# Optimization experiments

Measured on AMD Instinct MI355X. Metric: run time of the kernel, lower is better.

Reference implementation:

```python
import jax, jax.numpy as jnp
import numpy as np

T_INF = 10
LR_R = 0.02
EPS = 1e-5

def conv(x, w):
    # torch F.conv2d, padding=1, OIHW weights, NCHW data
    return jax.lax.conv_general_dilated(x, w, (1, 1), ((1, 1), (1, 1)),
                                        dimension_numbers=('NCHW', 'OIHW', 'NCHW'))

def convT(x, w):
    # torch ConvTranspose2d (stride=1, padding=1), weight layout (Cin, Cout, kH, kW)
    # equivalent to conv with spatially-flipped, channel-swapped kernel
    wc = jnp.flip(w, (2, 3)).transpose(1, 0, 2, 3)
    return conv(x, wc)

def maxpool2(x):
    return jax.lax.reduce_window(x, -jnp.inf, jax.lax.max, (1, 1, 2, 2), (1, 1, 2, 2), 'VALID')

def avgpool2(x):
    return jax.lax.reduce_window(x, 0.0, jax.lax.add, (1, 1, 2, 2), (1, 1, 2, 2), 'VALID') * 0.25

def bn(x, g, b):
    # BatchNorm2d in training mode (batch statistics, biased variance), eps=1e-5
    m = x.mean((0, 2, 3), keepdims=True)
    v = x.var((0, 2, 3), keepdims=True)
    return (x - m) * jax.lax.rsqrt(v + EPS) * g[None, :, None, None] + b[None, :, None, None]

def up2(x):
    return jnp.repeat(jnp.repeat(x, 2, axis=2), 2, axis=3)

def setup_inputs() -> dict:
    key = jax.random.key(0)
    B, C1, C2, C3 = 256, 64, 128, 256
    ks = jax.random.split(key, 12)
    def w(k, shape, fan_in):
        return jax.random.normal(k, shape, jnp.float32) * (1.0 / np.sqrt(fan_in))
    return {
        'x':  jax.random.normal(ks[0], (B, 3, 32, 32), jnp.float32),
        'W1': w(ks[1], (C1, 3, 3, 3), 3 * 9),
        'W2': w(ks[2], (C2, C1, 3, 3), C1 * 9),
        'W3': w(ks[3], (C3, C2, 3, 3), C2 * 9),
        'P2': w(ks[4], (C2, C1, 3, 3), C2 * 9),  # ConvTranspose2d(C2, C1) weight layout
        'P3': w(ks[5], (C3, C2, 3, 3), C3 * 9),  # ConvTranspose2d(C3, C2) weight layout
        'g1': jnp.ones((C1,), jnp.float32), 'b1': jnp.zeros((C1,), jnp.float32),
        'g2': jnp.ones((C2,), jnp.float32), 'b2': jnp.zeros((C2,), jnp.float32),
        'g3': jnp.ones((C3,), jnp.float32), 'b3': jnp.zeros((C3,), jnp.float32),
    }

def reference(x, W1, W2, W3, P2, P3, g1, b1, g2, b2, g3, b3):
    # feed-forward initialization
    r1 = maxpool2(jax.nn.relu(bn(conv(x, W1), g1, b1)))   # [B,C1,16,16]
    r2 = maxpool2(jax.nn.relu(bn(conv(r1, W2), g2, b2)))  # [B,C2,8,8]
    r3 = maxpool2(jax.nn.relu(bn(conv(r2, W3), g3, b3)))  # [B,C3,4,4]
    # iterative predictive-coding inference
    for _ in range(T_INF):
        pred1 = jnp.tanh(up2(convT(r2, P2)))  # P2(r2) is 8x8, upsample to 16x16
        pred2 = jnp.tanh(up2(convT(r3, P3)))  # P3(r3) is 4x4, upsample to 8x8
        e1 = r1 - pred1
        e2 = r2 - pred2
        dr1 = -e1
        dr2 = -e2 + avgpool2(conv(e1, W2))
        dr3 = avgpool2(conv(e2, W3))
        r1 = jax.nn.relu(r1 + LR_R * dr1)
        r2 = jax.nn.relu(r2 + LR_R * dr2)
        r3 = jax.nn.relu(r3 + LR_R * dr3)
    return (r1, r2, r3)
```

## Files before the change

kernel.cpp:

```cpp
#include <hip/hip_runtime.h>
#include <cstddef>
#include <cstdint>

#define LRr 0.02f

typedef unsigned short u16;
typedef __attribute__((ext_vector_type(8))) __bf16 bf16x8;
typedef __attribute__((ext_vector_type(8))) short short8;
typedef __attribute__((ext_vector_type(4))) float f32x4;
typedef __attribute__((ext_vector_type(4))) u16 u16x4;

static __device__ __forceinline__ u16 f2bf(float f) {
  union { float f; unsigned int u; } v{f};
  unsigned int r = (v.u + 0x7FFFu + ((v.u >> 16) & 1u)) >> 16;
  return (u16)r;
}
static __device__ __forceinline__ float bf2f(u16 h) {
  union { unsigned int u; float f; } v{(unsigned int)h << 16};
  return v.f;
}

static __device__ __forceinline__ void gload_lds16(const void* g, void* l) {
  __builtin_amdgcn_global_load_lds(
      (const __attribute__((address_space(1))) unsigned int*)g,
      (__attribute__((address_space(3))) unsigned int*)l, 16, 0, 0);
}

enum { EP_RAW = 0, EP_E1 = 1, EP_E2 = 2, EP_P2 = 3, EP_P3 = 4 };

template<int H, int CIN, int COUT, int WAVES_M, int WAVES_N, int WM, int WN,
         int NBLK, int EPI, bool SPLIT_M, bool STATS>
__device__ __forceinline__ void gemm_body(
    int bid, char* lds,
    const u16* __restrict__ in, const u16* __restrict__ wpk,
    float* __restrict__ fout, u16* __restrict__ bout,
    const u16* __restrict__ aux, float* __restrict__ sums)
{
  constexpr int P = H * H, W = H;
  constexpr int LW = (H == 16) ? 4 : ((H == 8) ? 3 : 2);
  constexpr int M_rep = WM / 16, N_rep = WN / 16;
  constexpr int CCH = CIN / 32;
  constexpr int PW = H + 2;
  constexpr int ALDS = PW * PW * CIN * 2;
  constexpr int COB = WAVES_N * WN;
  constexpr int BSTEP = 32 * COB * 2;
  constexpr int NS = 9 * CCH;
  static_assert(SPLIT_M ? (WAVES_M * WM * NBLK == P) : (WAVES_M * WM == P), "M");
  static_assert(SPLIT_M ? (COB == COUT) : (COB * NBLK == COUT), "N");
  static_assert(ALDS + 2 * BSTEP <= 64 * 1024, "lds");

  const int tid = threadIdx.x;
  const int l = tid & 63, l15 = l & 15, lq = l >> 4;
  const int wid = tid >> 6;
  const int wn = wid % WAVES_N, wm = wid / WAVES_N;

  const int img  = (NBLK == 1) ? bid : bid / NBLK;
  const int half = (NBLK == 1) ? 0 : bid % NBLK;
  const int pix0 = SPLIT_M ? half * (WAVES_M * WM) : 0;
  const int co0b = SPLIT_M ? 0 : half * COB;
  const int wm0  = pix0 + wm * WM;
  const int co   = co0b + wn * WN;

  auto stageB = [&](int buf, int step) {
    constexpr int ROUNDS = (4 * COB) / 256;
#pragma unroll
    for (int r = 0; r < ROUNDS; ++r) {
      int j = r * 256 + tid;
      int g = j / COB, c = j % COB;
      const char* gp = (const char*)wpk + ((size_t)((step * 4 + g) * COUT + co0b + c) << 4);
      char* lp = lds + ALDS + buf * BSTEP + ((r * 256 + (tid & 192)) << 4);
      gload_lds16(gp, lp);
    }
  };

  stageB(0, 0);
  for (int i = tid * 16; i < ALDS; i += 4096)
    *(int4*)(lds + i) = make_int4(0, 0, 0, 0);
  __syncthreads();
  constexpr int NCH = P * CIN / 8;
  for (int i = tid; i < NCH; i += 256) {
    int pix = i / (CIN / 8), c8 = i % (CIN / 8);
    const char* gp = (const char*)in + (((size_t)img * P + pix) * CIN + c8 * 8) * 2;
    int cell = ((pix >> LW) + 1) * PW + (pix & (W - 1)) + 1;
    int lb = ((cell * CIN + c8 * 8) << 1) ^ ((cell & 7) << 4);
    *(short8*)(lds + lb) = *(const short8*)gp;
  }
  __syncthreads();

  f32x4 acc[M_rep][N_rep];
#pragma unroll
  for (int m = 0; m < M_rep; ++m)
#pragma unroll
    for (int n = 0; n < N_rep; ++n)
#pragma unroll
      for (int r = 0; r < 4; ++r) acc[m][n][r] = 0.f;

  int ym[M_rep], xm[M_rep];
#pragma unroll
  for (int m = 0; m < M_rep; ++m) {
    int pix = wm0 + m * 16 + l15;
    ym[m] = pix >> LW;
    xm[m] = pix & (W - 1);
  }

  int step = 0, buf = 0;
  for (int tap = 0; tap < 9; ++tap) {
    const int dy = tap / 3, dx = tap % 3;
    for (int cc = 0; cc < CCH; ++cc) {
      if (step + 1 < NS) stageB(buf ^ 1, step + 1);
      bf16x8 af[M_rep], bfr[N_rep];
#pragma unroll
      for (int m = 0; m < M_rep; ++m) {
        int cell = (ym[m] + dy) * PW + xm[m] + dx;
        int lb = ((cell * CIN + cc * 32 + lq * 8) << 1) ^ ((cell & 7) << 4);
        af[m] = *(const bf16x8*)(lds + lb);
      }
#pragma unroll
      for (int n = 0; n < N_rep; ++n) {
        int lb = (lq * COB + wn * WN + n * 16 + l15) << 4;
        bfr[n] = *(const bf16x8*)(lds + ALDS + buf * BSTEP + lb);
      }
#pragma unroll
      for (int m = 0; m < M_rep; ++m)
#pragma unroll
        for (int n = 0; n < N_rep; ++n)
          acc[m][n] = __builtin_amdgcn_mfma_f32_16x16x32_bf16(af[m], bfr[n], acc[m][n], 0, 0, 0);
      __syncthreads();
      buf ^= 1;
      ++step;
    }
  }

  if constexpr (STATS) {
    float* sbuf = (float*)lds;
    for (int i = tid; i < 2 * COB; i += 256) sbuf[i] = 0.f;
    __syncthreads();
#pragma unroll
    for (int n = 0; n < N_rep; ++n) {
      float s1 = 0.f, s2 = 0.f;
#pragma unroll
      for (int m = 0; m < M_rep; ++m)
#pragma unroll
        for (int r = 0; r < 4; ++r) {
          float v = acc[m][n][r];
          s1 += v; s2 += v * v;
        }
      s1 += __shfl_xor(s1, 16); s2 += __shfl_xor(s2, 16);
      s1 += __shfl_xor(s1, 32); s2 += __shfl_xor(s2, 32);
      if (lq == 0) {
        int cg = wn * WN + n * 16 + l15;
        atomicAdd(&sbuf[2 * cg], s1);
        atomicAdd(&sbuf[2 * cg + 1], s2);
      }
    }
    __syncthreads();
    for (int i = tid; i < 2 * COB; i += 256) atomicAdd(&sums[2 * co0b + i], sbuf[i]);
  }

  const int gyx = 0; (void)gyx;

  if constexpr (EPI == EP_RAW) {
#pragma unroll
    for (int m = 0; m < M_rep; ++m)
#pragma unroll
      for (int n = 0; n < N_rep; ++n)
#pragma unroll
        for (int r = 0; r < 4; ++r) {
          int pix = wm0 + m * 16 + lq * 4 + r;
          bout[((size_t)img * P + pix) * COUT + co + n * 16 + l15] = f2bf(acc[m][n][r]);
        }
  } else if constexpr (EPI == EP_E1) {
#pragma unroll
    for (int m = 0; m < M_rep; ++m)
#pragma unroll
      for (int n = 0; n < N_rep; ++n)
#pragma unroll
        for (int r = 0; r < 4; ++r) {
          int pix = wm0 + m * 16 + lq * 4 + r;
          int y = pix >> 3, x = pix & 7;
          int cg = co + n * 16 + l15;
          float t = tanhf(acc[m][n][r]);
#pragma unroll
          for (int d2 = 0; d2 < 4; ++d2) {
            size_t idx = ((size_t)img * 256 + (2 * y + (d2 >> 1)) * 16 + 2 * x + (d2 & 1)) * 64 + cg;
            float rv = fout[idx];
            float e = rv - t;
            bout[idx] = f2bf(e);
            fout[idx] = fmaxf(rv - LRr * e, 0.f);
          }
        }
  } else if constexpr (EPI == EP_E2) {
#pragma unroll
    for (int n = 0; n < N_rep; ++n)
#pragma unroll
      for (int r = 0; r < 4; ++r) {
        int pix = lq * 4 + r;
        int y = pix >> 2, x = pix & 3;
        int cg = co + n * 16 + l15;
        float t = tanhf(acc[0][n][r]);
#pragma unroll
        for (int d2 = 0; d2 < 4; ++d2) {
          size_t idx = ((size_t)img * 64 + (2 * y + (d2 >> 1)) * 8 + 2 * x + (d2 & 1)) * 128 + cg;
          bout[idx] = f2bf(fout[idx] - t);
        }
      }
  } else if constexpr (EPI == EP_P2) {
#pragma unroll
    for (int m = 0; m < M_rep; m += 2)
#pragma unroll
      for (int n = 0; n < N_rep; ++n)
#pragma unroll
        for (int r0 = 0; r0 < 4; r0 += 2) {
          float sum = acc[m][n][r0] + acc[m][n][r0 + 1] + acc[m + 1][n][r0] + acc[m + 1][n][r0 + 1];
          int yo = ((wm0 >> 4) + m) >> 1;
          int xo = 2 * lq + (r0 >> 1);
          int cg = co + n * 16 + l15;
          size_t idx = ((size_t)img * 64 + yo * 8 + xo) * 128 + cg;
          float old = fout[idx];
          float d = 0.25f * sum - bf2f(aux[idx]);
          float nv = fmaxf(fmaf(LRr, d, old), 0.f);
          fout[idx] = nv;
          bout[idx] = f2bf(nv);
        }
  } else {
#pragma unroll
    for (int m = 0; m < M_rep; ++m)
#pragma unroll
      for (int n = 0; n < N_rep; ++n)
#pragma unroll
        for (int r0 = 0; r0 < 4; r0 += 2) {
          float sx = acc[m][n][r0] + acc[m][n][r0 + 1];
          float sum = sx + __shfl_xor(sx, 32);
          if (l < 32) {
            int yo = (wm0 >> 4) + m;
            int xo = 2 * (lq & 1) + (r0 >> 1);
            int cg = co + n * 16 + l15;
            size_t idx = ((size_t)img * 16 + yo * 4 + xo) * 256 + cg;
            float nv = fmaxf(fmaf(LRr, 0.25f * sum, fout[idx]), 0.f);
            fout[idx] = nv;
            bout[idx] = f2bf(nv);
          }
        }
  }
}

__global__ __launch_bounds__(256) void ff2_k(const u16* __restrict__ in, const u16* __restrict__ wpk,
                                             u16* __restrict__ outb, float* __restrict__ sums) {
  __shared__ __align__(16) char lds[49664];
  gemm_body<16, 64, 128, 4, 1, 64, 64, 2, EP_RAW, false, true>(
      blockIdx.x, lds, in, wpk, nullptr, outb, nullptr, sums);
}

__global__ __launch_bounds__(256) void ff3_k(const u16* __restrict__ in, const u16* __restrict__ wpk,
                                             u16* __restrict__ outb, float* __restrict__ sums) {
  __shared__ __align__(16) char lds[41984];
  gemm_body<8, 128, 256, 2, 2, 32, 64, 2, EP_RAW, false, true>(
      blockIdx.x, lds, in, wpk, nullptr, outb, nullptr, sums);
}

__global__ __launch_bounds__(256) void ea_k(const u16* __restrict__ r2b, const u16* __restrict__ P2pk,
                                            float* __restrict__ r1, u16* __restrict__ e1b,
                                            const u16* __restrict__ r3b, const u16* __restrict__ P3pk,
                                            const float* __restrict__ r2, u16* __restrict__ e2b) {
  __shared__ __align__(16) char lds[34816];
  if (blockIdx.x < 512)
    gemm_body<8, 128, 64, 2, 2, 16, 32, 2, EP_E1, true, false>(
        blockIdx.x, lds, r2b, P2pk, r1, e1b, nullptr, nullptr);
  else
    gemm_body<4, 256, 128, 1, 4, 16, 32, 1, EP_E2, false, false>(
        blockIdx.x - 512, lds, r3b, P3pk, (float*)r2, e2b, nullptr, nullptr);
}

__global__ __launch_bounds__(256) void pb_k(const u16* __restrict__ e1b, const u16* __restrict__ W2pk,
                                            float* __restrict__ r2, u16* __restrict__ r2b,
                                            const u16* __restrict__ e2b, const u16* __restrict__ W3pk,
                                            float* __restrict__ r3, u16* __restrict__ r3b) {
  __shared__ __align__(16) char lds[49664];
  if (blockIdx.x < 512)
    gemm_body<16, 64, 128, 4, 1, 64, 64, 2, EP_P2, false, false>(
        blockIdx.x, lds, e1b, W2pk, r2, r2b, e2b, nullptr);
  else
    gemm_body<8, 128, 256, 2, 2, 32, 64, 2, EP_P3, false, false>(
        blockIdx.x - 512, lds, e2b, W3pk, r3, r3b, nullptr, nullptr);
}

template<int CI, int CO, bool FLIP>
__global__ __launch_bounds__(256) void pack_k(const float* __restrict__ src, u16* __restrict__ dst) {
  int idx = blockIdx.x * 256 + threadIdx.x;
  int tap = idx / (CI * CO), rem = idx % (CI * CO);
  int ci = rem / CO, c = rem % CO;
  int dy = tap / 3, dx = tap % 3;
  float v = FLIP ? src[((size_t)ci * CO + c) * 9 + (2 - dy) * 3 + (2 - dx)]
                 : src[((size_t)c * CI + ci) * 9 + dy * 3 + dx];
  dst[(((size_t)tap * (CI / 8) + (ci >> 3)) * CO + c) * 8 + (ci & 7)] = f2bf(v);
}

__global__ __launch_bounds__(256) void conv1_k(const float* __restrict__ x,
                                               const float* __restrict__ W1,
                                               u16* __restrict__ t1,
                                               float* __restrict__ sums) {
  __shared__ float s[972];
  __shared__ float csum[16];
  const int bid = blockIdx.x;
  const int cog = bid & 7, tile = (bid >> 3) & 3, img = bid >> 5;
  const int ty0 = (tile >> 1) * 16, tx0 = (tile & 1) * 16;
  const int tid = threadIdx.x, ty = tid >> 4, tx = tid & 15;
  if (tid < 16) csum[tid] = 0.f;
  for (int i = tid; i < 972; i += 256) {
    int xx = i % 18, yy = (i / 18) % 18, cc = i / 324;
    int gy = ty0 + yy - 1, gx = tx0 + xx - 1;
    float v = 0.f;
    if (gy >= 0 && gy < 32 && gx >= 0 && gx < 32)
      v = x[((size_t)(img * 3 + cc) * 32 + gy) * 32 + gx];
    s[i] = v;
  }
  __syncthreads();
  float acc[8] = {};
#pragma unroll
  for (int cc = 0; cc < 3; ++cc)
#pragma unroll
    for (int dy = 0; dy < 3; ++dy)
#pragma unroll
      for (int dx = 0; dx < 3; ++dx) {
        float v = s[cc * 324 + (ty + dy) * 18 + tx + dx];
#pragma unroll
        for (int k = 0; k < 8; ++k)
          acc[k] = fmaf(v, W1[(((size_t)(cog * 8 + k) * 3 + cc) * 3 + dy) * 3 + dx], acc[k]);
      }
#pragma unroll
  for (int k = 0; k < 8; ++k) {
    float s1 = acc[k], s2 = acc[k] * acc[k];
#pragma unroll
    for (int off = 1; off < 64; off <<= 1) {
      s1 += __shfl_xor(s1, off);
      s2 += __shfl_xor(s2, off);
    }
    if ((tid & 63) == 0) {
      atomicAdd(&csum[2 * k], s1);
      atomicAdd(&csum[2 * k + 1], s2);
    }
  }
  short8 o;
#pragma unroll
  for (int k = 0; k < 8; ++k) o[k] = (short)f2bf(acc[k]);
  *(short8*)(t1 + ((size_t)img * 1024 + (ty0 + ty) * 32 + tx0 + tx) * 64 + cog * 8) = o;
  __syncthreads();
  if (tid < 16) atomicAdd(&sums[cog * 16 + tid], csum[tid]);
}

__global__ void ss_k(const float* __restrict__ sums, const float* __restrict__ g,
                     const float* __restrict__ b, float* __restrict__ ss, int C, float invN) {
  int c = blockIdx.x * 64 + threadIdx.x;
  if (c < C) {
    float m = sums[2 * c] * invN;
    float var = sums[2 * c + 1] * invN - m * m;
    float sc = g[c] * rsqrtf(var + 1e-5f);
    ss[c] = sc;
    ss[C + c] = b[c] - m * sc;
  }
}

template<int C, int H>
__global__ __launch_bounds__(256) void bnpool_k(const u16* __restrict__ t, const float* __restrict__ ss,
                                                float* __restrict__ r, u16* __restrict__ rb) {
  constexpr int HP = H / 2, C4 = C / 4;
  int idx = blockIdx.x * 256 + threadIdx.x;
  int c4 = idx % C4, po = idx / C4;
  int xo = po % HP, t2 = po / HP;
  int yo = t2 % HP, img = t2 / HP;
  const u16* p0 = t + (((size_t)img * H + 2 * yo) * H + 2 * xo) * C + c4 * 4;
  u16x4 a = *(const u16x4*)p0, b = *(const u16x4*)(p0 + C);
  u16x4 c_ = *(const u16x4*)(p0 + H * C), d = *(const u16x4*)(p0 + H * C + C);
  f32x4 sc = *(const f32x4*)(ss + c4 * 4);
  f32x4 sh = *(const f32x4*)(ss + C + c4 * 4);
  f32x4 o;
#pragma unroll
  for (int j = 0; j < 4; ++j) {
    float v0 = fmaf(bf2f(a[j]), sc[j], sh[j]);
    float v1 = fmaf(bf2f(b[j]), sc[j], sh[j]);
    float v2 = fmaf(bf2f(c_[j]), sc[j], sh[j]);
    float v3 = fmaf(bf2f(d[j]), sc[j], sh[j]);
    o[j] = fmaxf(fmaxf(fmaxf(v0, v1), fmaxf(v2, v3)), 0.f);
  }
  *(f32x4*)(r + (size_t)idx * 4) = o;
  u16x4 ob;
#pragma unroll
  for (int j = 0; j < 4; ++j) ob[j] = f2bf(o[j]);
  *(u16x4*)(rb + (size_t)idx * 4) = ob;
}

template<int P, int C, int CHUNKS>
__global__ __launch_bounds__(256) void tr_k(const float* __restrict__ in, float* __restrict__ out) {
  constexpr int TP = P / CHUNKS;
  __shared__ float tl[TP][C + 1];
  const int img = blockIdx.x, ch = blockIdx.y;
  const float* ip = in + (size_t)img * P * C;
  float* op = out + (size_t)img * P * C;
  for (int i = threadIdx.x; i < TP * C / 4; i += 256) {
    int p = i / (C / 4), c4 = i % (C / 4);
    f32x4 v = *(const f32x4*)&ip[(size_t)(ch * TP + p) * C + c4 * 4];
#pragma unroll
    for (int j = 0; j < 4; ++j) tl[p][c4 * 4 + j] = v[j];
  }
  __syncthreads();
  for (int i = threadIdx.x; i < TP * C; i += 256) {
    int c = i / TP, p = i % TP;
    op[(size_t)c * P + ch * TP + p] = tl[p][c];
  }
}

extern "C" void kernel_launch(void* const* d_in, const int* in_sizes, int n_in,
                              void* d_out, int out_size, void* d_ws, size_t ws_size,
                              hipStream_t stream) {
  const float* x  = (const float*)d_in[0];
  const float* W1 = (const float*)d_in[1];
  const float* W2 = (const float*)d_in[2];
  const float* W3 = (const float*)d_in[3];
  const float* P2 = (const float*)d_in[4];
  const float* P3 = (const float*)d_in[5];
  const float* g1 = (const float*)d_in[6];
  const float* b1 = (const float*)d_in[7];
  const float* g2 = (const float*)d_in[8];
  const float* b2 = (const float*)d_in[9];
  const float* g3 = (const float*)d_in[10];
  const float* b3 = (const float*)d_in[11];

  char* w = (char*)d_ws;
  auto alloc = [&](size_t n) { char* p = w; w += (n + 255) & ~(size_t)255; return p; };
  float* r1  = (float*)alloc(16777216);
  float* r2  = (float*)alloc(8388608);
  float* r3  = (float*)alloc(4194304);
  u16* r1b   = (u16*)alloc(8388608);
  u16* r2b   = (u16*)alloc(4194304);
  u16* r3b   = (u16*)alloc(2097152);
  u16* W2pk  = (u16*)alloc(147456);
  u16* W3pk  = (u16*)alloc(589824);
  u16* P2pk  = (u16*)alloc(147456);
  u16* P3pk  = (u16*)alloc(589824);
  float* sums = (float*)alloc(3584);
  float* ssb  = (float*)alloc(3584);
  char* S = alloc(33554432);
  u16* t1 = (u16*)S;
  u16* t2 = (u16*)S;
  u16* t3 = (u16*)S;
  u16* e1b = (u16*)S;
  u16* e2b = (u16*)(S + 8388608);

  hipMemsetAsync(sums, 0, 3584, stream);

  pack_k<64, 128, false><<<288, 256, 0, stream>>>(W2, W2pk);
  pack_k<128, 256, false><<<1152, 256, 0, stream>>>(W3, W3pk);
  pack_k<128, 64, true><<<288, 256, 0, stream>>>(P2, P2pk);
  pack_k<256, 128, true><<<1152, 256, 0, stream>>>(P3, P3pk);

  conv1_k<<<8192, 256, 0, stream>>>(x, W1, t1, sums);
  ss_k<<<1, 64, 0, stream>>>(sums, g1, b1, ssb, 64, 1.f / 262144.f);
  bnpool_k<64, 32><<<4096, 256, 0, stream>>>(t1, ssb, r1, r1b);

  ff2_k<<<512, 256, 0, stream>>>(r1b, W2pk, t2, sums + 128);
  ss_k<<<2, 64, 0, stream>>>(sums + 128, g2, b2, ssb + 128, 128, 1.f / 65536.f);
  bnpool_k<128, 16><<<2048, 256, 0, stream>>>(t2, ssb + 128, r2, r2b);

  ff3_k<<<512, 256, 0, stream>>>(r2b, W3pk, t3, sums + 384);
  ss_k<<<4, 64, 0, stream>>>(sums + 384, g3, b3, ssb + 384, 256, 1.f / 16384.f);
  bnpool_k<256, 8><<<1024, 256, 0, stream>>>(t3, ssb + 384, r3, r3b);

  for (int it = 0; it < 10; ++it) {
    ea_k<<<768, 256, 0, stream>>>(r2b, P2pk, r1, e1b, r3b, P3pk, r2, e2b);
    pb_k<<<1024, 256, 0, stream>>>(e1b, W2pk, r2, r2b, e2b, W3pk, r3, r3b);
  }

  float* out = (float*)d_out;
  tr_k<256, 64, 4><<<dim3(256, 4), 256, 0, stream>>>(r1, out);
  tr_k<64, 128, 1><<<dim3(256, 1), 256, 0, stream>>>(r2, out + 4194304);
  tr_k<16, 256, 1><<<dim3(256, 1), 256, 0, stream>>>(r3, out + 6291456);
}
```

Measured before the change: 803.1 us.

## Read conv activations from global memory, stage per-tap weights, recompute conv1 via MFMA

The shared implicit-GEMM body no longer copies a zero-padded activation tile into LDS. A-fragments are loaded straight from global memory with bounds masks, and a whole tap of weights is double-buffered in LDS, so there is one barrier per tap instead of one per channel chunk. Block/wave splits change for the error and update kernels. Conv1 becomes an MFMA kernel run twice, once for BN statistics and once fused with BN+ReLU+maxpool, which removes the bf16 t1 intermediate and the separate bnpool pass. The cost is uncached, uncoalesced-per-lane global loads in the inner loop and a larger LDS footprint that may cut occupancy.

Result: slower. 1.072 ms (+33.5%).

```diff
diff --git a/kernel.cpp b/kernel.cpp
--- a/kernel.cpp
+++ b/kernel.cpp
@@ -28,8 +28,8 @@
 
 enum { EP_RAW = 0, EP_E1 = 1, EP_E2 = 2, EP_P2 = 3, EP_P3 = 4 };
 
-template<int H, int CIN, int COUT, int WAVES_M, int WAVES_N, int WM, int WN,
-         int NBLK, int EPI, bool SPLIT_M, bool STATS>
+template<int H, int CIN, int COUT, int WAVES_M, int WAVES_N, int WN, int NBLK,
+         int EPI, bool STATS>
 __device__ __forceinline__ void gemm_body(
     int bid, char* lds,
     const u16* __restrict__ in, const u16* __restrict__ wpk,
@@ -38,54 +38,37 @@
 {
   constexpr int P = H * H, W = H;
   constexpr int LW = (H == 16) ? 4 : ((H == 8) ? 3 : 2);
+  constexpr int WM = P / WAVES_M;
   constexpr int M_rep = WM / 16, N_rep = WN / 16;
   constexpr int CCH = CIN / 32;
-  constexpr int PW = H + 2;
-  constexpr int ALDS = PW * PW * CIN * 2;
   constexpr int COB = WAVES_N * WN;
-  constexpr int BSTEP = 32 * COB * 2;
-  constexpr int NS = 9 * CCH;
-  static_assert(SPLIT_M ? (WAVES_M * WM * NBLK == P) : (WAVES_M * WM == P), "M");
-  static_assert(SPLIT_M ? (COB == COUT) : (COB * NBLK == COUT), "N");
-  static_assert(ALDS + 2 * BSTEP <= 64 * 1024, "lds");
+  constexpr int BTAP = CIN * COB * 2;
+  constexpr int ROUNDS = (BTAP / 16) / 256;
+  static_assert((BTAP / 16) % 256 == 0, "g");
+  static_assert(COB * NBLK == COUT, "n");
+  static_assert(WAVES_M * WAVES_N == 4, "w");
 
   const int tid = threadIdx.x;
   const int l = tid & 63, l15 = l & 15, lq = l >> 4;
   const int wid = tid >> 6;
   const int wn = wid % WAVES_N, wm = wid / WAVES_N;
-
-  const int img  = (NBLK == 1) ? bid : bid / NBLK;
-  const int half = (NBLK == 1) ? 0 : bid % NBLK;
-  const int pix0 = SPLIT_M ? half * (WAVES_M * WM) : 0;
-  const int co0b = SPLIT_M ? 0 : half * COB;
-  const int wm0  = pix0 + wm * WM;
-  const int co   = co0b + wn * WN;
-
-  auto stageB = [&](int buf, int step) {
-    constexpr int ROUNDS = (4 * COB) / 256;
+  const int img = bid / NBLK, half = bid % NBLK;
+  const int co0b = half * COB;
+  const int wm0 = wm * WM;
+  const int co = co0b + wn * WN;
+  const u16* Ain = in + (size_t)img * P * CIN;
+
+  auto stageB = [&](int buf, int tap) {
 #pragma unroll
     for (int r = 0; r < ROUNDS; ++r) {
       int j = r * 256 + tid;
-      int g = j / COB, c = j % COB;
-      const char* gp = (const char*)wpk + ((size_t)((step * 4 + g) * COUT + co0b + c) << 4);
-      char* lp = lds + ALDS + buf * BSTEP + ((r * 256 + (tid & 192)) << 4);
+      int ci8 = j / COB, c = j % COB;
+      const char* gp = (const char*)wpk +
+          ((size_t)((tap * (CIN / 8) + ci8) * COUT + co0b + c) << 4);
+      char* lp = lds + buf * BTAP + ((r * 256 + (tid & 192)) << 4);
       gload_lds16(gp, lp);
     }
   };
-
-  stageB(0, 0);
-  for (int i = tid * 16; i < ALDS; i += 4096)
-    *(int4*)(lds + i) = make_int4(0, 0, 0, 0);
-  __syncthreads();
-  constexpr int NCH = P * CIN / 8;
-  for (int i = tid; i < NCH; i += 256) {
-    int pix = i / (CIN / 8), c8 = i % (CIN / 8);
-    const char* gp = (const char*)in + (((size_t)img * P + pix) * CIN + c8 * 8) * 2;
-    int cell = ((pix >> LW) + 1) * PW + (pix & (W - 1)) + 1;
-    int lb = ((cell * CIN + c8 * 8) << 1) ^ ((cell & 7) << 4);
-    *(short8*)(lds + lb) = *(const short8*)gp;
-  }
-  __syncthreads();
 
   f32x4 acc[M_rep][N_rep];
 #pragma unroll
@@ -103,32 +86,40 @@
     xm[m] = pix & (W - 1);
   }
 
-  int step = 0, buf = 0;
+  stageB(0, 0);
+  __syncthreads();
+  int buf = 0;
   for (int tap = 0; tap < 9; ++tap) {
-    const int dy = tap / 3, dx = tap % 3;
+    const int dy = tap / 3 - 1, dx = tap % 3 - 1;
+    if (tap < 8) stageB(buf ^ 1, tap + 1);
+    int sp[M_rep]; bool av[M_rep];
+#pragma unroll
+    for (int m = 0; m < M_rep; ++m) {
+      int sy = ym[m] + dy, sx = xm[m] + dx;
+      av[m] = ((unsigned)sy < (unsigned)H) & ((unsigned)sx < (unsigned)W);
+      sp[m] = sy * W + sx;
+    }
+#pragma unroll
     for (int cc = 0; cc < CCH; ++cc) {
-      if (step + 1 < NS) stageB(buf ^ 1, step + 1);
       bf16x8 af[M_rep], bfr[N_rep];
 #pragma unroll
       for (int m = 0; m < M_rep; ++m) {
-        int cell = (ym[m] + dy) * PW + xm[m] + dx;
-        int lb = ((cell * CIN + cc * 32 + lq * 8) << 1) ^ ((cell & 7) << 4);
-        af[m] = *(const bf16x8*)(lds + lb);
+        short8 t{};
+        if (av[m]) t = *(const short8*)(Ain + sp[m] * CIN + cc * 32 + lq * 8);
+        af[m] = __builtin_bit_cast(bf16x8, t);
       }
 #pragma unroll
-      for (int n = 0; n < N_rep; ++n) {
-        int lb = (lq * COB + wn * WN + n * 16 + l15) << 4;
-        bfr[n] = *(const bf16x8*)(lds + ALDS + buf * BSTEP + lb);
-      }
+      for (int n = 0; n < N_rep; ++n)
+        bfr[n] = *(const bf16x8*)(lds + buf * BTAP +
+                   (((cc * 4 + lq) * COB + wn * WN + n * 16 + l15) << 4));
 #pragma unroll
       for (int m = 0; m < M_rep; ++m)
 #pragma unroll
         for (int n = 0; n < N_rep; ++n)
           acc[m][n] = __builtin_amdgcn_mfma_f32_16x16x32_bf16(af[m], bfr[n], acc[m][n], 0, 0, 0);
-      __syncthreads();
-      buf ^= 1;
-      ++step;
-    }
+    }
+    __syncthreads();
+    buf ^= 1;
   }
 
   if constexpr (STATS) {
@@ -141,10 +132,7 @@
 #pragma unroll
       for (int m = 0; m < M_rep; ++m)
 #pragma unroll
-        for (int r = 0; r < 4; ++r) {
-          float v = acc[m][n][r];
-          s1 += v; s2 += v * v;
-        }
+        for (int r = 0; r < 4; ++r) { float v = acc[m][n][r]; s1 += v; s2 += v * v; }
       s1 += __shfl_xor(s1, 16); s2 += __shfl_xor(s2, 16);
       s1 += __shfl_xor(s1, 32); s2 += __shfl_xor(s2, 32);
       if (lq == 0) {
@@ -156,8 +144,6 @@
     __syncthreads();
     for (int i = tid; i < 2 * COB; i += 256) atomicAdd(&sums[2 * co0b + i], sbuf[i]);
   }
-
-  const int gyx = 0; (void)gyx;
 
   if constexpr (EPI == EP_RAW) {
 #pragma unroll
@@ -246,42 +232,36 @@
 
 __global__ __launch_bounds__(256) void ff2_k(const u16* __restrict__ in, const u16* __restrict__ wpk,
                                              u16* __restrict__ outb, float* __restrict__ sums) {
-  __shared__ __align__(16) char lds[49664];
-  gemm_body<16, 64, 128, 4, 1, 64, 64, 2, EP_RAW, false, true>(
-      blockIdx.x, lds, in, wpk, nullptr, outb, nullptr, sums);
+  __shared__ __align__(16) char lds[16384];
+  gemm_body<16, 64, 128, 4, 1, 64, 2, EP_RAW, true>(blockIdx.x, lds, in, wpk, nullptr, outb, nullptr, sums);
 }
 
 __global__ __launch_bounds__(256) void ff3_k(const u16* __restrict__ in, const u16* __restrict__ wpk,
                                              u16* __restrict__ outb, float* __restrict__ sums) {
-  __shared__ __align__(16) char lds[41984];
-  gemm_body<8, 128, 256, 2, 2, 32, 64, 2, EP_RAW, false, true>(
-      blockIdx.x, lds, in, wpk, nullptr, outb, nullptr, sums);
+  __shared__ __align__(16) char lds[65536];
+  gemm_body<8, 128, 256, 2, 2, 64, 2, EP_RAW, true>(blockIdx.x, lds, in, wpk, nullptr, outb, nullptr, sums);
 }
 
 __global__ __launch_bounds__(256) void ea_k(const u16* __restrict__ r2b, const u16* __restrict__ P2pk,
                                             float* __restrict__ r1, u16* __restrict__ e1b,
                                             const u16* __restrict__ r3b, const u16* __restrict__ P3pk,
                                             const float* __restrict__ r2, u16* __restrict__ e2b) {
-  __shared__ __align__(16) char lds[34816];
-  if (blockIdx.x < 512)
-    gemm_body<8, 128, 64, 2, 2, 16, 32, 2, EP_E1, true, false>(
-        blockIdx.x, lds, r2b, P2pk, r1, e1b, nullptr, nullptr);
+  __shared__ __align__(16) char lds[65536];
+  if (blockIdx.x < 256)
+    gemm_body<8, 128, 64, 2, 2, 32, 1, EP_E1, false>(blockIdx.x, lds, r2b, P2pk, r1, e1b, nullptr, nullptr);
   else
-    gemm_body<4, 256, 128, 1, 4, 16, 32, 1, EP_E2, false, false>(
-        blockIdx.x - 512, lds, r3b, P3pk, (float*)r2, e2b, nullptr, nullptr);
+    gemm_body<4, 256, 128, 1, 4, 16, 2, EP_E2, false>(blockIdx.x - 256, lds, r3b, P3pk, (float*)r2, e2b, nullptr, nullptr);
 }
 
 __global__ __launch_bounds__(256) void pb_k(const u16* __restrict__ e1b, const u16* __restrict__ W2pk,
                                             float* __restrict__ r2, u16* __restrict__ r2b,
                                             const u16* __restrict__ e2b, const u16* __restrict__ W3pk,
                                             float* __restrict__ r3, u16* __restrict__ r3b) {
-  __shared__ __align__(16) char lds[49664];
+  __shared__ __align__(16) char lds[65536];
   if (blockIdx.x < 512)
-    gemm_body<16, 64, 128, 4, 1, 64, 64, 2, EP_P2, false, false>(
-        blockIdx.x, lds, e1b, W2pk, r2, r2b, e2b, nullptr);
+    gemm_body<16, 64, 128, 4, 1, 64, 2, EP_P2, false>(blockIdx.x, lds, e1b, W2pk, r2, r2b, e2b, nullptr);
   else
-    gemm_body<8, 128, 256, 2, 2, 32, 64, 2, EP_P3, false, false>(
-        blockIdx.x - 512, lds, e2b, W3pk, r3, r3b, nullptr, nullptr);
+    gemm_body<8, 128, 256, 2, 2, 64, 2, EP_P3, false>(blockIdx.x - 512, lds, e2b, W3pk, r3, r3b, nullptr, nullptr);
 }
 
 template<int CI, int CO, bool FLIP>
@@ -295,57 +275,129 @@
   dst[(((size_t)tap * (CI / 8) + (ci >> 3)) * CO + c) * 8 + (ci & 7)] = f2bf(v);
 }
 
-__global__ __launch_bounds__(256) void conv1_k(const float* __restrict__ x,
-                                               const float* __restrict__ W1,
-                                               u16* __restrict__ t1,
-                                               float* __restrict__ sums) {
-  __shared__ float s[972];
-  __shared__ float csum[16];
+__global__ void pack1_k(const float* __restrict__ W1, u16* __restrict__ W1pk) {
+  for (int j = threadIdx.x; j < 2048; j += 256) {
+    int klo = j & 7, rest = j >> 3;
+    int co = rest & 63, k8 = rest >> 6;
+    int k = k8 * 8 + klo;
+    float v = 0.f;
+    if (k < 27) {
+      int tap = k / 3, cc = k % 3, dy = tap / 3, dx = tap % 3;
+      v = W1[((size_t)(co * 3 + cc) * 3 + dy) * 3 + dx];
+    }
+    W1pk[j] = f2bf(v);
+  }
+}
+
+template<bool POOL>
+__global__ __launch_bounds__(256) void c1_k(const float* __restrict__ x,
+                                            const u16* __restrict__ W1pk,
+                                            float* __restrict__ sums,
+                                            const float* __restrict__ ss,
+                                            float* __restrict__ r1,
+                                            u16* __restrict__ r1b) {
+  __shared__ __align__(16) char lds[28480];
+  float* xs = (float*)lds;
+  char* Al = lds + 3904;
+  char* Bl = lds + 3904 + 20480;
   const int bid = blockIdx.x;
-  const int cog = bid & 7, tile = (bid >> 3) & 3, img = bid >> 5;
-  const int ty0 = (tile >> 1) * 16, tx0 = (tile & 1) * 16;
-  const int tid = threadIdx.x, ty = tid >> 4, tx = tid & 15;
-  if (tid < 16) csum[tid] = 0.f;
+  const int img = bid >> 2, quad = bid & 3;
+  const int ty0 = (quad >> 1) * 16, tx0 = (quad & 1) * 16;
+  const int tid = threadIdx.x;
+  const int l = tid & 63, l15 = l & 15, lq = l >> 4;
+  const int wm = tid >> 6;
+
+  gload_lds16((const char*)W1pk + tid * 16, Bl + ((tid & 192) << 4));
   for (int i = tid; i < 972; i += 256) {
     int xx = i % 18, yy = (i / 18) % 18, cc = i / 324;
     int gy = ty0 + yy - 1, gx = tx0 + xx - 1;
     float v = 0.f;
     if (gy >= 0 && gy < 32 && gx >= 0 && gx < 32)
       v = x[((size_t)(img * 3 + cc) * 32 + gy) * 32 + gx];
-    s[i] = v;
+    xs[i] = v;
   }
   __syncthreads();
-  float acc[8] = {};
-#pragma unroll
-  for (int cc = 0; cc < 3; ++cc)
-#pragma unroll
-    for (int dy = 0; dy < 3; ++dy)
-#pragma unroll
-      for (int dx = 0; dx < 3; ++dx) {
-        float v = s[cc * 324 + (ty + dy) * 18 + tx + dx];
-#pragma unroll
-        for (int k = 0; k < 8; ++k)
-          acc[k] = fmaf(v, W1[(((size_t)(cog * 8 + k) * 3 + cc) * 3 + dy) * 3 + dx], acc[k]);
+  {
+    int ty = tid >> 4, tx = tid & 15;
+    u16 a[32];
+#pragma unroll
+    for (int tap = 0; tap < 9; ++tap)
+#pragma unroll
+      for (int cc = 0; cc < 3; ++cc)
+        a[tap * 3 + cc] = f2bf(xs[cc * 324 + (ty + tap / 3) * 18 + tx + tap % 3]);
+#pragma unroll
+    for (int k = 27; k < 32; ++k) a[k] = 0;
+#pragma unroll
+    for (int i = 0; i < 4; ++i)
+      *(short8*)(Al + tid * 80 + i * 16) = *(short8*)&a[i * 8];
+  }
+  __syncthreads();
+
+  f32x4 acc[4][4];
+  bf16x8 af[4], bfr[4];
+#pragma unroll
+  for (int m = 0; m < 4; ++m) {
+    int pix = wm * 64 + m * 16 + l15;
+    af[m] = *(const bf16x8*)(Al + pix * 80 + lq * 16);
+  }
+#pragma unroll
+  for (int n = 0; n < 4; ++n)
+    bfr[n] = *(const bf16x8*)(Bl + ((lq * 64 + n * 16 + l15) << 4));
+#pragma unroll
+  for (int m = 0; m < 4; ++m)
+#pragma unroll
+    for (int n = 0; n < 4; ++n) {
+      f32x4 z = {0.f, 0.f, 0.f, 0.f};
+      acc[m][n] = __builtin_amdgcn_mfma_f32_16x16x32_bf16(af[m], bfr[n], z, 0, 0, 0);
+    }
+
+  if constexpr (!POOL) {
+    float* sbuf = (float*)lds;
+    __syncthreads();
+    for (int i = tid; i < 128; i += 256) sbuf[i] = 0.f;
+    __syncthreads();
+#pragma unroll
+    for (int n = 0; n < 4; ++n) {
+      float s1 = 0.f, s2 = 0.f;
+#pragma unroll
+      for (int m = 0; m < 4; ++m)
+#pragma unroll
+        for (int r = 0; r < 4; ++r) { float v = acc[m][n][r]; s1 += v; s2 += v * v; }
+      s1 += __shfl_xor(s1, 16); s2 += __shfl_xor(s2, 16);
+      s1 += __shfl_xor(s1, 32); s2 += __shfl_xor(s2, 32);
+      if (lq == 0) {
+        int cg = n * 16 + l15;
+        atomicAdd(&sbuf[2 * cg], s1);
+        atomicAdd(&sbuf[2 * cg + 1], s2);
       }
-#pragma unroll
-  for (int k = 0; k < 8; ++k) {
-    float s1 = acc[k], s2 = acc[k] * acc[k];
-#pragma unroll
-    for (int off = 1; off < 64; off <<= 1) {
-      s1 += __shfl_xor(s1, off);
-      s2 += __shfl_xor(s2, off);
-    }
-    if ((tid & 63) == 0) {
-      atomicAdd(&csum[2 * k], s1);
-      atomicAdd(&csum[2 * k + 1], s2);
-    }
-  }
-  short8 o;
-#pragma unroll
-  for (int k = 0; k < 8; ++k) o[k] = (short)f2bf(acc[k]);
-  *(short8*)(t1 + ((size_t)img * 1024 + (ty0 + ty) * 32 + tx0 + tx) * 64 + cog * 8) = o;
-  __syncthreads();
-  if (tid < 16) atomicAdd(&sums[cog * 16 + tid], csum[tid]);
+    }
+    __syncthreads();
+    if (tid < 128) atomicAdd(&sums[tid], sbuf[tid]);
+  } else {
+    float ssv[4], ssh[4];
+#pragma unroll
+    for (int n = 0; n < 4; ++n) {
+      ssv[n] = ss[n * 16 + l15];
+      ssh[n] = ss[64 + n * 16 + l15];
+    }
+#pragma unroll
+    for (int m = 0; m < 4; m += 2)
+#pragma unroll
+      for (int n = 0; n < 4; ++n)
+#pragma unroll
+        for (int r0 = 0; r0 < 4; r0 += 2) {
+          float a0 = fmaf(acc[m][n][r0], ssv[n], ssh[n]);
+          float a1 = fmaf(acc[m][n][r0 + 1], ssv[n], ssh[n]);
+          float b0 = fmaf(acc[m + 1][n][r0], ssv[n], ssh[n]);
+          float b1 = fmaf(acc[m + 1][n][r0 + 1], ssv[n], ssh[n]);
+          float v = fmaxf(fmaxf(fmaxf(a0, a1), fmaxf(b0, b1)), 0.f);
+          int py = (ty0 >> 1) + ((wm * 4 + m) >> 1);
+          int px = (tx0 >> 1) + ((lq * 4 + r0) >> 1);
+          size_t idx = ((size_t)img * 256 + py * 16 + px) * 64 + n * 16 + l15;
+          r1[idx] = v;
+          r1b[idx] = f2bf(v);
+        }
+  }
 }
 
 __global__ void ss_k(const float* __restrict__ sums, const float* __restrict__ g,
@@ -437,10 +489,10 @@
   u16* W3pk  = (u16*)alloc(589824);
   u16* P2pk  = (u16*)alloc(147456);
   u16* P3pk  = (u16*)alloc(589824);
+  u16* W1pk  = (u16*)alloc(4096);
   float* sums = (float*)alloc(3584);
   float* ssb  = (float*)alloc(3584);
   char* S = alloc(33554432);
-  u16* t1 = (u16*)S;
   u16* t2 = (u16*)S;
   u16* t3 = (u16*)S;
   u16* e1b = (u16*)S;
@@ -452,10 +504,11 @@
   pack_k<128, 256, false><<<1152, 256, 0, stream>>>(W3, W3pk);
   pack_k<128, 64, true><<<288, 256, 0, stream>>>(P2, P2pk);
   pack_k<256, 128, true><<<1152, 256, 0, stream>>>(P3, P3pk);
-
-  conv1_k<<<8192, 256, 0, stream>>>(x, W1, t1, sums);
+  pack1_k<<<1, 256, 0, stream>>>(W1, W1pk);
+
+  c1_k<false><<<1024, 256, 0, stream>>>(x, W1pk, sums, nullptr, nullptr, nullptr);
   ss_k<<<1, 64, 0, stream>>>(sums, g1, b1, ssb, 64, 1.f / 262144.f);
-  bnpool_k<64, 32><<<4096, 256, 0, stream>>>(t1, ssb, r1, r1b);
+  c1_k<true><<<1024, 256, 0, stream>>>(x, W1pk, nullptr, ssb, r1, r1b);
 
   ff2_k<<<512, 256, 0, stream>>>(r1b, W2pk, t2, sums + 128);
   ss_k<<<2, 64, 0, stream>>>(sums + 128, g2, b2, ssb + 128, 128, 1.f / 65536.f);
```
